# Optimization experiments

Hardware: AMD Instinct MI355X
Metric: run time of the kernel (lower is better)

## Reference

```python
import jax, jax.numpy as jnp
import numpy as np

B, S, D, H = 4, 2048, 512, 8
HD = D // H
POOL_HEADS = 8


def setup_inputs() -> dict:
    key = jax.random.key(0)
    ks = iter(jax.random.split(key, 32))
    p = {}
    p['x'] = jax.random.normal(next(ks), (B, S, D), dtype=jnp.float32)
    p['mask'] = jnp.zeros((B, S), dtype=jnp.float32)  # key_padding_mask (1.0 = padded)
    s = 1.0 / np.sqrt(D)
    for layer in ('1', '2'):
        for name in ('q', 'k', 'v', 'o'):
            p[f'{name}{layer}_w'] = jax.random.normal(next(ks), (D, D), dtype=jnp.float32) * s
            p[f'{name}{layer}_b'] = jnp.zeros((D,), dtype=jnp.float32)
    p['ln1_g'] = jnp.ones((D,), jnp.float32); p['ln1_b'] = jnp.zeros((D,), jnp.float32)
    p['ffn_w1'] = jax.random.normal(next(ks), (D, D), dtype=jnp.float32) * s
    p['ffn_b1'] = jnp.zeros((D,), jnp.float32)
    p['ffn_w2'] = jax.random.normal(next(ks), (D, D), dtype=jnp.float32) * s
    p['ffn_b2'] = jnp.zeros((D,), jnp.float32)
    p['ln2_g'] = jnp.ones((D,), jnp.float32); p['ln2_b'] = jnp.zeros((D,), jnp.float32)
    p['pool_w'] = jax.random.normal(next(ks), (D, POOL_HEADS), dtype=jnp.float32) * s
    p['pool_b'] = jnp.zeros((POOL_HEADS,), jnp.float32)
    return p


def _layernorm(x, g, b, eps=1e-5):
    mu = jnp.mean(x, axis=-1, keepdims=True)
    var = jnp.var(x, axis=-1, keepdims=True)
    return (x - mu) * jax.lax.rsqrt(var + eps) * g + b


def _mha(x, mask, qw, qb, kw, kb, vw, vb, ow, ob):
    b, s, d = x.shape
    q = (x @ qw + qb).reshape(b, s, H, HD)
    k = (x @ kw + kb).reshape(b, s, H, HD)
    v = (x @ vw + vb).reshape(b, s, H, HD)
    scores = jnp.einsum('bihd,bjhd->bhij', q, k) / jnp.sqrt(jnp.float32(HD))
    scores = scores - mask[:, None, None, :] * 1e30  # key_padding_mask
    w = jax.nn.softmax(scores, axis=-1)  # dropout is identity at eval
    out = jnp.einsum('bhij,bjhd->bihd', w, v).reshape(b, s, d)
    return out @ ow + ob


def _pool(x, mask, pw, pb):
    alpha = jax.nn.leaky_relu(x @ pw + pb)            # [B,S,POOL_HEADS]
    alpha = alpha + mask[:, :, None] * -1e16
    alpha = jax.nn.softmax(alpha, axis=1)             # softmax over sequence
    # sum over heads of alpha_h * x, then sum over sequence
    return jnp.einsum('bs,bsd->bd', alpha.sum(axis=-1), x)


def reference(x, mask,
              q1_w, q1_b, k1_w, k1_b, v1_w, v1_b, o1_w, o1_b,
              q2_w, q2_b, k2_w, k2_b, v2_w, v2_b, o2_w, o2_b,
              ln1_g, ln1_b, ffn_w1, ffn_b1, ffn_w2, ffn_b2,
              ln2_g, ln2_b, pool_w, pool_b):
    # F.normalize(x, p=2, dim=-1)
    x = x / jnp.maximum(jnp.linalg.norm(x, axis=-1, keepdims=True), 1e-12)
    h = _mha(x, mask, q1_w, q1_b, k1_w, k1_b, v1_w, v1_b, o1_w, o1_b)
    h = _layernorm(h, ln1_g, ln1_b)
    h = jax.nn.relu(h @ ffn_w1 + ffn_b1) @ ffn_w2 + ffn_b2
    h = _mha(h, mask, q2_w, q2_b, k2_w, k2_b, v2_w, v2_b, o2_w, o2_b)
    h = _layernorm(h, ln2_g, ln2_b)
    return _pool(h, mask, pool_w, pool_b)  # [B, D] patch_feature (cls=False -> logit is None)
```

## Files before the change

kernel.cpp:

```cpp
#include <hip/hip_runtime.h>
#include <hip/hip_bf16.h>
#include <stdint.h>

#define DEVI __device__ __forceinline__

typedef float f32x4 __attribute__((ext_vector_type(4)));
typedef short bf16x8 __attribute__((ext_vector_type(8)));

typedef __attribute__((address_space(3))) unsigned int as3_u32;
typedef __attribute__((address_space(1))) unsigned int as1_u32;

DEVI void gload16(const void* g, void* l) {
  __builtin_amdgcn_global_load_lds((const as1_u32*)g, (as3_u32*)l, 16, 0, 0);
}

DEVI unsigned short bf16r(float f) {
  union { float f; unsigned int u; } v; v.f = f;
  unsigned int u = v.u;
  return (unsigned short)((u + 0x7FFFu + ((u >> 16) & 1u)) >> 16);
}

DEVI float bf2f(unsigned short u) {
  unsigned int x = ((unsigned int)u) << 16;
  union { unsigned int u; float f; } v; v.u = x;
  return v.f;
}

struct PrepArgs {
  const float* w[10];
  const float* b1[3];
  const float* b2[3];
};

__global__ __launch_bounds__(256) void prep_kernel(PrepArgs pa, unsigned short* wt,
                                                   float* qb1, float* qb2) {
  __shared__ float lt[64][65];
  const int slot = blockIdx.z;
  const int n0 = blockIdx.x * 64, k0 = blockIdx.y * 64;
  const float* W = pa.w[slot];
  for (int it = 0; it < 16; it++) {
    int idx = it * 256 + threadIdx.x;
    int kr = idx >> 6, nc = idx & 63;
    lt[kr][nc] = W[(long)(k0 + kr) * 512 + n0 + nc];
  }
  __syncthreads();
  unsigned short* dst = wt + (long)slot * 512 * 512;
  for (int it = 0; it < 16; it++) {
    int idx = it * 256 + threadIdx.x;
    int nr = idx >> 6, kc = idx & 63;
    dst[(long)(n0 + nr) * 512 + k0 + kc] = bf16r(lt[kc][nr]);
  }
  if (blockIdx.x == 0 && blockIdx.y == 0) {
    if (slot < 3) {
      for (int i = threadIdx.x; i < 512; i += 256) qb1[slot * 512 + i] = pa.b1[slot][i];
    } else if (slot >= 6 && slot < 9) {
      for (int i = threadIdx.x; i < 512; i += 256) qb2[(slot - 6) * 512 + i] = pa.b2[slot - 6][i];
    }
  }
}

__global__ __launch_bounds__(256) void l2norm_kernel(const float* __restrict__ x,
                                                     unsigned short* __restrict__ xn) {
  const long row = blockIdx.x;
  const float* xr = x + row * 512;
  float v0 = xr[threadIdx.x], v1 = xr[threadIdx.x + 256];
  float ss = v0 * v0 + v1 * v1;
  #pragma unroll
  for (int off = 32; off > 0; off >>= 1) ss += __shfl_down(ss, off, 64);
  __shared__ float red[4];
  __shared__ float sc[1];
  int w = threadIdx.x >> 6, ln = threadIdx.x & 63;
  if (ln == 0) red[w] = ss;
  __syncthreads();
  if (threadIdx.x == 0) {
    float S = red[0] + red[1] + red[2] + red[3];
    sc[0] = 1.0f / fmaxf(sqrtf(S), 1e-12f);
  }
  __syncthreads();
  float s = sc[0];
  xn[row * 512 + threadIdx.x] = bf16r(v0 * s);
  xn[row * 512 + threadIdx.x + 256] = bf16r(v1 * s);
}

template <int EPI>
__global__ __launch_bounds__(256) void gemm_bt(const unsigned short* __restrict__ A,
                                               const unsigned short* __restrict__ Bt,
                                               const float* __restrict__ bias,
                                               void* __restrict__ Cv, int K, int N,
                                               unsigned short* __restrict__ vtout) {
  __shared__ unsigned short ldsA[128 * 64];
  __shared__ unsigned short ldsB[128 * 64];
  const int tid = threadIdx.x, w = tid >> 6, ln = tid & 63;
  const int bm = blockIdx.x, bn = blockIdx.y;
  const int wm = (w >> 1) * 64, wn = (w & 1) * 64;
  const f32x4 zf = {0.f, 0.f, 0.f, 0.f};
  f32x4 acc[4][4];
  #pragma unroll
  for (int i = 0; i < 4; i++)
    #pragma unroll
    for (int j = 0; j < 4; j++) acc[i][j] = zf;
  const int r8 = ln >> 3, s8 = ln & 7;
  for (int kt = 0; kt < K; kt += 64) {
    #pragma unroll
    for (int i = 0; i < 4; i++) {
      int row = w * 32 + i * 8 + r8;
      gload16(A + (long)(bm * 128 + row) * K + kt + s8 * 8, &ldsA[(w * 32 + i * 8) * 64]);
      gload16(Bt + (long)(bn * 128 + row) * K + kt + s8 * 8, &ldsB[(w * 32 + i * 8) * 64]);
    }
    __syncthreads();
    #pragma unroll
    for (int kk = 0; kk < 2; kk++) {
      bf16x8 af[4], bfr[4];
      #pragma unroll
      for (int mf = 0; mf < 4; mf++) {
        int row = wm + mf * 16 + (ln & 15);
        af[mf] = *(const bf16x8*)&ldsA[row * 64 + kk * 32 + (ln >> 4) * 8];
      }
      #pragma unroll
      for (int nf = 0; nf < 4; nf++) {
        int row = wn + nf * 16 + (ln & 15);
        bfr[nf] = *(const bf16x8*)&ldsB[row * 64 + kk * 32 + (ln >> 4) * 8];
      }
      #pragma unroll
      for (int mf = 0; mf < 4; mf++)
        #pragma unroll
        for (int nf = 0; nf < 4; nf++)
          acc[mf][nf] = __builtin_amdgcn_mfma_f32_16x16x32_bf16(af[mf], bfr[nf], acc[mf][nf], 0, 0, 0);
    }
    __syncthreads();
  }
  const int g = ln >> 4, c = ln & 15;
  #pragma unroll
  for (int mf = 0; mf < 4; mf++) {
    #pragma unroll
    for (int nf = 0; nf < 4; nf++) {
      int col = bn * 128 + wn + nf * 16 + c;
      float bv = bias[col];
      if (EPI == 3 && col >= 1024) {
        long row0 = bm * 128 + wm + mf * 16 + g * 4;
        int b = (int)(row0 >> 11), s = (int)(row0 & 2047);
        int vc = col - 1024, h = vc >> 6, hd = vc & 63;
        ushort4 o;
        o.x = bf16r(acc[mf][nf][0] + bv);
        o.y = bf16r(acc[mf][nf][1] + bv);
        o.z = bf16r(acc[mf][nf][2] + bv);
        o.w = bf16r(acc[mf][nf][3] + bv);
        *(ushort4*)(vtout + ((long)((b * 8 + h) * 64 + hd)) * 2048 + s) = o;
      } else {
        #pragma unroll
        for (int j = 0; j < 4; j++) {
          long row = bm * 128 + wm + mf * 16 + g * 4 + j;
          float v = acc[mf][nf][j] + bv;
          if (EPI == 2) v = v > 0.f ? v : 0.f;
          if (EPI == 0)
            ((float*)Cv)[row * N + col] = v;
          else
            ((unsigned short*)Cv)[row * N + col] = bf16r(v);
        }
      }
    }
  }
}

template <int EPI>
__global__ __launch_bounds__(256) void gemm_bt64(const unsigned short* __restrict__ A,
                                                 const unsigned short* __restrict__ Bt,
                                                 const float* __restrict__ bias,
                                                 void* __restrict__ Cv, int K, int N) {
  __shared__ unsigned short ldsA[128 * 64];
  __shared__ unsigned short ldsB[64 * 64];
  const int tid = threadIdx.x, w = tid >> 6, ln = tid & 63;
  const int bm = blockIdx.x, bn = blockIdx.y;
  const int wm = (w >> 1) * 64, wn = (w & 1) * 32;
  const f32x4 zf = {0.f, 0.f, 0.f, 0.f};
  f32x4 acc[4][2];
  #pragma unroll
  for (int i = 0; i < 4; i++)
    #pragma unroll
    for (int j = 0; j < 2; j++) acc[i][j] = zf;
  const int r8 = ln >> 3, s8 = ln & 7;
  for (int kt = 0; kt < K; kt += 64) {
    #pragma unroll
    for (int i = 0; i < 6; i++) {
      int jj = w * 6 + i;
      if (jj < 16) {
        gload16(A + (long)(bm * 128 + jj * 8 + r8) * K + kt + s8 * 8, &ldsA[jj * 512]);
      } else {
        int jb = jj - 16;
        gload16(Bt + (long)(bn * 64 + jb * 8 + r8) * K + kt + s8 * 8, &ldsB[jb * 512]);
      }
    }
    __syncthreads();
    #pragma unroll
    for (int kk = 0; kk < 2; kk++) {
      bf16x8 af[4], bfr[2];
      #pragma unroll
      for (int mf = 0; mf < 4; mf++)
        af[mf] = *(const bf16x8*)&ldsA[(wm + mf * 16 + (ln & 15)) * 64 + kk * 32 + (ln >> 4) * 8];
      #pragma unroll
      for (int nf = 0; nf < 2; nf++)
        bfr[nf] = *(const bf16x8*)&ldsB[(wn + nf * 16 + (ln & 15)) * 64 + kk * 32 + (ln >> 4) * 8];
      #pragma unroll
      for (int mf = 0; mf < 4; mf++)
        #pragma unroll
        for (int nf = 0; nf < 2; nf++)
          acc[mf][nf] = __builtin_amdgcn_mfma_f32_16x16x32_bf16(af[mf], bfr[nf], acc[mf][nf], 0, 0, 0);
    }
    __syncthreads();
  }
  const int g = ln >> 4, c = ln & 15;
  #pragma unroll
  for (int mf = 0; mf < 4; mf++) {
    #pragma unroll
    for (int nf = 0; nf < 2; nf++) {
      int col = bn * 64 + wn + nf * 16 + c;
      float bv = bias[col];
      #pragma unroll
      for (int j = 0; j < 4; j++) {
        long row = bm * 128 + wm + mf * 16 + g * 4 + j;
        float v = acc[mf][nf][j] + bv;
        if (EPI == 2) v = v > 0.f ? v : 0.f;
        if (EPI == 0)
          ((float*)Cv)[row * N + col] = v;
        else
          ((unsigned short*)Cv)[row * N + col] = bf16r(v);
      }
    }
  }
}

__global__ __launch_bounds__(256, 4) void attn_split_kernel(
    const unsigned short* __restrict__ qkv,
    const unsigned short* __restrict__ vt,
    const float* __restrict__ mask,
    unsigned short* __restrict__ opart,
    float* __restrict__ lpart) {
  const int tid = threadIdx.x, w = tid >> 6, ln = tid & 63;
  const int g = ln >> 4, c = ln & 15;
  const int bh = blockIdx.y, b = bh >> 3, h = bh & 7;
  const int sp = blockIdx.z;
  const int q0 = blockIdx.x * 128 + w * 32;
  const unsigned short* qp = qkv + (long)(b * 2048) * 1536 + h * 64;
  const unsigned short* kp = qp + 512;
  const unsigned short* vtp = vt + (long)bh * 64 * 2048;
  const float* mp = mask + b * 2048;

  __shared__ unsigned short kbuf[2][32 * 64];
  __shared__ unsigned short vbuf[2][64 * 32];
  __shared__ unsigned short pbuf[4 * 16 * 64];
  unsigned short* pb = &pbuf[w * 1024];

  const int jj0 = w * 2;
  auto stage = [&](int buf, int kt) {
    #pragma unroll
    for (int u = 0; u < 2; u++) {
      int jj = jj0 + u;
      if (jj < 4) {
        int r = jj * 8 + (ln >> 3);
        int s = ln & 7;
        gload16(kp + (long)(kt + r) * 1536 + ((s ^ (r & 7)) * 8),
                &kbuf[buf][jj * 512]);
      } else {
        int j = jj - 4;
        int r = j * 16 + (ln >> 2);
        int s = ln & 3;
        gload16(vtp + (long)r * 2048 + kt + ((s ^ ((r >> 1) & 3)) * 8),
                &vbuf[buf][j * 512]);
      }
    }
  };

  const f32x4 zf = {0.f, 0.f, 0.f, 0.f};
  bf16x8 qf[2][2];
  #pragma unroll
  for (int qi = 0; qi < 2; qi++)
    #pragma unroll
    for (int kk = 0; kk < 2; kk++)
      qf[qi][kk] = *(const bf16x8*)(qp + (long)(q0 + qi * 16 + c) * 1536 + kk * 32 + g * 8);

  f32x4 of[4][2];
  #pragma unroll
  for (int i = 0; i < 4; i++)
    #pragma unroll
    for (int j = 0; j < 2; j++) of[i][j] = zf;
  float lsum[2] = {0.f, 0.f};

  const int kt0 = sp * 1024;
  stage(0, kt0);
  __syncthreads();

  for (int it = 0; it < 32; it++) {
    const int kt = kt0 + it * 32;
    const int cur = it & 1;
    if (it + 1 < 32) stage(cur ^ 1, kt + 32);
    float mval = mp[kt + (ln & 31)];
    bf16x8 kf[2][2];
    #pragma unroll
    for (int ki = 0; ki < 2; ki++)
      #pragma unroll
      for (int kk = 0; kk < 2; kk++)
        kf[ki][kk] = *(const bf16x8*)&kbuf[cur][(ki * 16 + c) * 64 + (((kk * 4 + g) ^ (c & 7)) * 8)];
    bf16x8 vf[4];
    #pragma unroll
    for (int hf = 0; hf < 4; hf++)
      vf[hf] = *(const bf16x8*)&vbuf[cur][(hf * 16 + c) * 32 + ((g ^ ((c >> 1) & 3)) * 8)];
    f32x4 st[2][2];
    #pragma unroll
    for (int ki = 0; ki < 2; ki++)
      #pragma unroll
      for (int qi = 0; qi < 2; qi++) {
        f32x4 t0 = __builtin_amdgcn_mfma_f32_16x16x32_bf16(kf[ki][0], qf[qi][0], zf, 0, 0, 0);
        st[ki][qi] = __builtin_amdgcn_mfma_f32_16x16x32_bf16(kf[ki][1], qf[qi][1], t0, 0, 0, 0);
      }
    float madj[2][4];
    #pragma unroll
    for (int ki = 0; ki < 2; ki++)
      #pragma unroll
      for (int j = 0; j < 4; j++) madj[ki][j] = 0.f;
    if (__any(mval != 0.f)) {
      #pragma unroll
      for (int ki = 0; ki < 2; ki++)
        #pragma unroll
        for (int j = 0; j < 4; j++)
          madj[ki][j] = -1.4426950408889634e30f * __shfl(mval, ki * 16 + g * 4 + j, 64);
    }
    const float SC = 0.18033688011112042f;
    #pragma unroll
    for (int qi = 0; qi < 2; qi++) {
      #pragma unroll
      for (int ki = 0; ki < 2; ki++) {
        float e0 = __builtin_amdgcn_exp2f(st[ki][qi][0] * SC + madj[ki][0]);
        float e1 = __builtin_amdgcn_exp2f(st[ki][qi][1] * SC + madj[ki][1]);
        float e2 = __builtin_amdgcn_exp2f(st[ki][qi][2] * SC + madj[ki][2]);
        float e3 = __builtin_amdgcn_exp2f(st[ki][qi][3] * SC + madj[ki][3]);
        lsum[qi] += (e0 + e1) + (e2 + e3);
        __hip_bfloat162 h01 = __float22bfloat162_rn(make_float2(e0, e1));
        __hip_bfloat162 h23 = __float22bfloat162_rn(make_float2(e2, e3));
        uint2 pk;
        pk.x = *(unsigned int*)&h01;
        pk.y = *(unsigned int*)&h23;
        int slot = (qi * 4 + ki * 2 + (g >> 1)) ^ (c & 7);
        *(uint2*)&pb[c * 64 + slot * 8 + (g & 1) * 4] = pk;
      }
    }
    bf16x8 pfr[2];
    #pragma unroll
    for (int qi = 0; qi < 2; qi++) {
      int slot = (qi * 4 + g) ^ (c & 7);
      pfr[qi] = *(const bf16x8*)&pb[c * 64 + slot * 8];
    }
    #pragma unroll
    for (int hf = 0; hf < 4; hf++)
      #pragma unroll
      for (int qi = 0; qi < 2; qi++)
        of[hf][qi] = __builtin_amdgcn_mfma_f32_16x16x32_bf16(vf[hf], pfr[qi], of[hf][qi], 0, 0, 0);
    __syncthreads();
  }
  #pragma unroll
  for (int qi = 0; qi < 2; qi++) {
    lsum[qi] += __shfl_xor(lsum[qi], 16, 64);
    lsum[qi] += __shfl_xor(lsum[qi], 32, 64);
  }
  unsigned short* ob = opart + (long)(sp * 32 + bh) * 2048 * 64;
  #pragma unroll
  for (int qi = 0; qi < 2; qi++) {
    long row = q0 + qi * 16 + c;
    #pragma unroll
    for (int hf = 0; hf < 4; hf++) {
      ushort4 o;
      o.x = bf16r(of[hf][qi][0]);
      o.y = bf16r(of[hf][qi][1]);
      o.z = bf16r(of[hf][qi][2]);
      o.w = bf16r(of[hf][qi][3]);
      *(ushort4*)(ob + row * 64 + hf * 16 + g * 4) = o;
    }
  }
  if (g == 0) {
    #pragma unroll
    for (int qi = 0; qi < 2; qi++)
      lpart[(long)(sp * 32 + bh) * 2048 + q0 + qi * 16 + c] = lsum[qi];
  }
}

__global__ __launch_bounds__(256) void attn_combine(const unsigned short* __restrict__ opart,
                                                    const float* __restrict__ lpart,
                                                    unsigned short* __restrict__ ao) {
  const long row = blockIdx.x;
  const int b = (int)(row >> 11), q = (int)(row & 2047);
  #pragma unroll
  for (int half = 0; half < 2; half++) {
    int col = threadIdx.x + half * 256;
    int h = col >> 6, hd = col & 63;
    int bh = b * 8 + h;
    float l = lpart[(long)bh * 2048 + q] + lpart[(long)(32 + bh) * 2048 + q];
    long i0 = ((long)bh * 2048 + q) * 64 + hd;
    long i1 = ((long)(32 + bh) * 2048 + q) * 64 + hd;
    float v = (bf2f(opart[i0]) + bf2f(opart[i1])) / l;
    ao[row * 512 + col] = bf16r(v);
  }
}

template <int OUTF>
__global__ __launch_bounds__(256) void ln_kernel(const float* __restrict__ in,
                                                 const float* __restrict__ gam,
                                                 const float* __restrict__ bet,
                                                 void* __restrict__ out) {
  const long row = blockIdx.x;
  const float* x = in + row * 512;
  float v0 = x[threadIdx.x], v1 = x[threadIdx.x + 256];
  float s = v0 + v1, ss = v0 * v0 + v1 * v1;
  #pragma unroll
  for (int off = 32; off > 0; off >>= 1) {
    s += __shfl_down(s, off, 64);
    ss += __shfl_down(ss, off, 64);
  }
  __shared__ float red[8];
  __shared__ float mv[2];
  int w = threadIdx.x >> 6, ln = threadIdx.x & 63;
  if (ln == 0) { red[w] = s; red[w + 4] = ss; }
  __syncthreads();
  if (threadIdx.x == 0) {
    float S = red[0] + red[1] + red[2] + red[3];
    float SS = red[4] + red[5] + red[6] + red[7];
    float mu = S * (1.f / 512.f);
    float var = SS * (1.f / 512.f) - mu * mu;
    mv[0] = mu;
    mv[1] = rsqrtf(var + 1e-5f);
  }
  __syncthreads();
  float mu = mv[0], rs = mv[1];
  float o0 = (v0 - mu) * rs * gam[threadIdx.x] + bet[threadIdx.x];
  float o1 = (v1 - mu) * rs * gam[threadIdx.x + 256] + bet[threadIdx.x + 256];
  if (OUTF == 0) {
    ((unsigned short*)out)[row * 512 + threadIdx.x] = bf16r(o0);
    ((unsigned short*)out)[row * 512 + threadIdx.x + 256] = bf16r(o1);
  } else {
    ((float*)out)[row * 512 + threadIdx.x] = o0;
    ((float*)out)[row * 512 + threadIdx.x + 256] = o1;
  }
}

__global__ __launch_bounds__(256) void alpha_kernel(const float* __restrict__ h,
                                                    const float* __restrict__ pw,
                                                    const float* __restrict__ pbias,
                                                    const float* __restrict__ mask,
                                                    float* __restrict__ alpha) {
  int w = threadIdx.x >> 6, ln = threadIdx.x & 63;
  long row = (long)blockIdx.x * 4 + w;
  float p[8];
  #pragma unroll
  for (int k = 0; k < 8; k++) p[k] = 0.f;
  #pragma unroll
  for (int it = 0; it < 8; it++) {
    int d = it * 64 + ln;
    float xv = h[row * 512 + d];
    const float* wr = pw + d * 8;
    #pragma unroll
    for (int k = 0; k < 8; k++) p[k] += xv * wr[k];
  }
  #pragma unroll
  for (int off = 32; off > 0; off >>= 1)
    #pragma unroll
    for (int k = 0; k < 8; k++) p[k] += __shfl_down(p[k], off, 64);
  if (ln == 0) {
    float mterm = mask[row] * (-1e16f);
    #pragma unroll
    for (int k = 0; k < 8; k++) {
      float a = p[k] + pbias[k];
      a = a < 0.f ? 0.01f * a : a;
      alpha[row * 8 + k] = a + mterm;
    }
  }
}

__global__ __launch_bounds__(256) void stats_kernel(const float* __restrict__ alpha,
                                                    float* __restrict__ stats) {
  int b = blockIdx.x >> 3, ph = blockIdx.x & 7;
  const float* a = alpha + (long)b * 2048 * 8 + ph;
  __shared__ float rr[4];
  __shared__ float mm[1];
  int w = threadIdx.x >> 6, ln = threadIdx.x & 63;
  float m = -1e38f;
  for (int s = threadIdx.x; s < 2048; s += 256) m = fmaxf(m, a[(long)s * 8]);
  #pragma unroll
  for (int off = 32; off > 0; off >>= 1) m = fmaxf(m, __shfl_down(m, off, 64));
  if (ln == 0) rr[w] = m;
  __syncthreads();
  if (threadIdx.x == 0) mm[0] = fmaxf(fmaxf(rr[0], rr[1]), fmaxf(rr[2], rr[3]));
  __syncthreads();
  float M = mm[0];
  float sum = 0.f;
  for (int s = threadIdx.x; s < 2048; s += 256) sum += __expf(a[(long)s * 8] - M);
  #pragma unroll
  for (int off = 32; off > 0; off >>= 1) sum += __shfl_down(sum, off, 64);
  __syncthreads();
  if (ln == 0) rr[w] = sum;
  __syncthreads();
  if (threadIdx.x == 0) {
    stats[blockIdx.x * 2] = M;
    stats[blockIdx.x * 2 + 1] = rr[0] + rr[1] + rr[2] + rr[3];
  }
}

__global__ __launch_bounds__(256) void pool_kernel(const float* __restrict__ h,
                                                   const float* __restrict__ alpha,
                                                   const float* __restrict__ stats,
                                                   float* __restrict__ partial) {
  int b = blockIdx.x >> 3, sc = blockIdx.x & 7;
  int s0 = sc * 256;
  __shared__ float wb[256];
  {
    long s = s0 + threadIdx.x;
    const float* a = alpha + ((long)b * 2048 + s) * 8;
    float wsum = 0.f;
    #pragma unroll
    for (int ph = 0; ph < 8; ph++) {
      float M = stats[(b * 8 + ph) * 2], Sm = stats[(b * 8 + ph) * 2 + 1];
      wsum += __expf(a[ph] - M) / Sm;
    }
    wb[threadIdx.x] = wsum;
  }
  __syncthreads();
  float a0 = 0.f, a1 = 0.f;
  const float* hb = h + ((long)b * 2048 + s0) * 512;
  for (int i = 0; i < 256; i++) {
    float wv = wb[i];
    a0 += wv * hb[(long)i * 512 + threadIdx.x];
    a1 += wv * hb[(long)i * 512 + threadIdx.x + 256];
  }
  partial[(long)blockIdx.x * 512 + threadIdx.x] = a0;
  partial[(long)blockIdx.x * 512 + threadIdx.x + 256] = a1;
}

__global__ __launch_bounds__(256) void pool_final(const float* __restrict__ partial,
                                                  float* __restrict__ out) {
  int b = blockIdx.x;
  float a0 = 0.f, a1 = 0.f;
  #pragma unroll
  for (int sc = 0; sc < 8; sc++) {
    a0 += partial[(long)(b * 8 + sc) * 512 + threadIdx.x];
    a1 += partial[(long)(b * 8 + sc) * 512 + threadIdx.x + 256];
  }
  out[b * 512 + threadIdx.x] = a0;
  out[b * 512 + threadIdx.x + 256] = a1;
}

extern "C" void kernel_launch(void* const* d_in, const int* in_sizes, int n_in,
                              void* d_out, int out_size, void* d_ws, size_t ws_size,
                              hipStream_t stream) {
  (void)in_sizes; (void)n_in; (void)out_size;
  if (ws_size < 92274688UL) return;

  const float* x    = (const float*)d_in[0];
  const float* mask = (const float*)d_in[1];
  const float* q1w = (const float*)d_in[2];  const float* q1b = (const float*)d_in[3];
  const float* k1w = (const float*)d_in[4];  const float* k1b = (const float*)d_in[5];
  const float* v1w = (const float*)d_in[6];  const float* v1b = (const float*)d_in[7];
  const float* o1w = (const float*)d_in[8];  const float* o1b = (const float*)d_in[9];
  const float* q2w = (const float*)d_in[10]; const float* q2b = (const float*)d_in[11];
  const float* k2w = (const float*)d_in[12]; const float* k2b = (const float*)d_in[13];
  const float* v2w = (const float*)d_in[14]; const float* v2b = (const float*)d_in[15];
  const float* o2w = (const float*)d_in[16]; const float* o2b = (const float*)d_in[17];
  const float* ln1g = (const float*)d_in[18]; const float* ln1b = (const float*)d_in[19];
  const float* fw1 = (const float*)d_in[20]; const float* fb1 = (const float*)d_in[21];
  const float* fw2 = (const float*)d_in[22]; const float* fb2 = (const float*)d_in[23];
  const float* ln2g = (const float*)d_in[24]; const float* ln2b = (const float*)d_in[25];
  const float* poolw = (const float*)d_in[26]; const float* poolb = (const float*)d_in[27];

  char* ws = (char*)d_ws;
  unsigned short* Wt  = (unsigned short*)(ws + 0);
  float* qb1          = (float*)(ws + 5242880);
  float* qb2          = (float*)(ws + 5249024);
  float* stats        = (float*)(ws + 5255168);
  float* alpha        = (float*)(ws + 5255424);
  float* partial      = (float*)(ws + 5517568);
  unsigned short* qkv = (unsigned short*)(ws + 8388608);
  unsigned short* vt  = (unsigned short*)(ws + 33554432);
  unsigned short* ao  = (unsigned short*)(ws + 41943040);
  float* t            = (float*)(ws + 50331648);
  unsigned short* xn  = (unsigned short*)(ws + 67108864);
  unsigned short* h1  = (unsigned short*)(ws + 75497472);
  unsigned short* f   = (unsigned short*)(ws + 83886080);
  unsigned short* h2  = xn;
  unsigned short* opart = (unsigned short*)(ws + 50331648);
  float* lpart          = (float*)(ws + 83886080);

  PrepArgs pa;
  pa.w[0] = q1w; pa.w[1] = k1w; pa.w[2] = v1w; pa.w[3] = o1w; pa.w[4] = fw1;
  pa.w[5] = fw2; pa.w[6] = q2w; pa.w[7] = k2w; pa.w[8] = v2w; pa.w[9] = o2w;
  pa.b1[0] = q1b; pa.b1[1] = k1b; pa.b1[2] = v1b;
  pa.b2[0] = q2b; pa.b2[1] = k2b; pa.b2[2] = v2b;

  prep_kernel<<<dim3(8, 8, 10), 256, 0, stream>>>(pa, Wt, qb1, qb2);
  l2norm_kernel<<<8192, 256, 0, stream>>>(x, xn);

  gemm_bt<3><<<dim3(64, 12), 256, 0, stream>>>(xn, Wt, qb1, qkv, 512, 1536, vt);
  attn_split_kernel<<<dim3(16, 32, 2), 256, 0, stream>>>(qkv, vt, mask, opart, lpart);
  attn_combine<<<8192, 256, 0, stream>>>(opart, lpart, ao);
  gemm_bt64<0><<<dim3(64, 8), 256, 0, stream>>>(ao, Wt + 3L * 512 * 512, o1b, t, 512, 512);
  ln_kernel<0><<<8192, 256, 0, stream>>>(t, ln1g, ln1b, h1);
  gemm_bt64<2><<<dim3(64, 8), 256, 0, stream>>>(h1, Wt + 4L * 512 * 512, fb1, f, 512, 512);
  gemm_bt64<1><<<dim3(64, 8), 256, 0, stream>>>(f, Wt + 5L * 512 * 512, fb2, h2, 512, 512);

  gemm_bt<3><<<dim3(64, 12), 256, 0, stream>>>(h2, Wt + 6L * 512 * 512, qb2, qkv, 512, 1536, vt);
  attn_split_kernel<<<dim3(16, 32, 2), 256, 0, stream>>>(qkv, vt, mask, opart, lpart);
  attn_combine<<<8192, 256, 0, stream>>>(opart, lpart, ao);
  gemm_bt64<0><<<dim3(64, 8), 256, 0, stream>>>(ao, Wt + 9L * 512 * 512, o2b, t, 512, 512);
  ln_kernel<1><<<8192, 256, 0, stream>>>(t, ln2g, ln2b, t);

  alpha_kernel<<<2048, 256, 0, stream>>>(t, poolw, poolb, mask, alpha);
  stats_kernel<<<32, 256, 0, stream>>>(alpha, stats);
  pool_kernel<<<32, 256, 0, stream>>>(t, alpha, stats, partial);
  pool_final<<<4, 256, 0, stream>>>(partial, (float*)d_out);
}
```

Measured before the change: 302.8 us.

## Switch split attention to 32x32x16 MFMA with register P exchange and block swizzle

Rewrites the attention inner loop to use 32x32x16 bf16 MFMA tiles instead of 16x16x32 ones, so each wave computes a 32x32 score tile in four MFMAs. The softmax probabilities are moved into B-operand layout with cross-half lane shuffles instead of a round trip through the per-wave LDS P buffer, which removes that shared memory and its writes and reads. It also remaps block IDs so consecutive blocks spread across heads and splits, which may improve L2 locality. The cost is larger accumulator register footprint (two 16-wide accumulators plus the score tile), which may pressure occupancy under the 4-block launch bound.

New measurement: 306.9 us. Within noise of the previous version (+1.3%).

```diff
diff --git a/kernel.cpp b/kernel.cpp
--- a/kernel.cpp
+++ b/kernel.cpp
@@ -5,6 +5,7 @@
 #define DEVI __device__ __forceinline__
 
 typedef float f32x4 __attribute__((ext_vector_type(4)));
+typedef float f32x16 __attribute__((ext_vector_type(16)));
 typedef short bf16x8 __attribute__((ext_vector_type(8)));
 
 typedef __attribute__((address_space(3))) unsigned int as3_u32;
@@ -24,6 +25,11 @@
   unsigned int x = ((unsigned int)u) << 16;
   union { unsigned int u; float f; } v; v.u = x;
   return v.f;
+}
+
+DEVI unsigned int pkbf16(float a, float b) {
+  __hip_bfloat162 h = __float22bfloat162_rn(make_float2(a, b));
+  return *(unsigned int*)&h;
 }
 
 struct PrepArgs {
@@ -236,10 +242,12 @@
     unsigned short* __restrict__ opart,
     float* __restrict__ lpart) {
   const int tid = threadIdx.x, w = tid >> 6, ln = tid & 63;
-  const int g = ln >> 4, c = ln & 15;
-  const int bh = blockIdx.y, b = bh >> 3, h = bh & 7;
-  const int sp = blockIdx.z;
-  const int q0 = blockIdx.x * 128 + w * 32;
+  const int lo = ln & 31, hi = ln >> 5;
+  const int bid = blockIdx.x + 16 * blockIdx.y + 512 * blockIdx.z;
+  const int swz = (bid & 7) * 128 + (bid >> 3);
+  const int qb = swz & 15, bh = (swz >> 4) & 31, sp = swz >> 9;
+  const int b = bh >> 3, h = bh & 7;
+  const int q0 = qb * 128 + w * 32;
   const unsigned short* qp = qkv + (long)(b * 2048) * 1536 + h * 64;
   const unsigned short* kp = qp + 512;
   const unsigned short* vtp = vt + (long)bh * 64 * 2048;
@@ -247,8 +255,6 @@
 
   __shared__ unsigned short kbuf[2][32 * 64];
   __shared__ unsigned short vbuf[2][64 * 32];
-  __shared__ unsigned short pbuf[4 * 16 * 64];
-  unsigned short* pb = &pbuf[w * 1024];
 
   const int jj0 = w * 2;
   auto stage = [&](int buf, int kt) {
@@ -270,20 +276,18 @@
     }
   };
 
-  const f32x4 zf = {0.f, 0.f, 0.f, 0.f};
-  bf16x8 qf[2][2];
-  #pragma unroll
-  for (int qi = 0; qi < 2; qi++)
-    #pragma unroll
-    for (int kk = 0; kk < 2; kk++)
-      qf[qi][kk] = *(const bf16x8*)(qp + (long)(q0 + qi * 16 + c) * 1536 + kk * 32 + g * 8);
-
-  f32x4 of[4][2];
-  #pragma unroll
-  for (int i = 0; i < 4; i++)
-    #pragma unroll
-    for (int j = 0; j < 2; j++) of[i][j] = zf;
-  float lsum[2] = {0.f, 0.f};
+  bf16x8 qf[4];
+  #pragma unroll
+  for (int t = 0; t < 4; t++)
+    qf[t] = *(const bf16x8*)(qp + (long)(q0 + lo) * 1536 + t * 16 + hi * 8);
+
+  f32x16 oacc[2];
+  #pragma unroll
+  for (int t = 0; t < 2; t++)
+    #pragma unroll
+    for (int r = 0; r < 16; r++) oacc[t][r] = 0.f;
+  float lsum = 0.f;
+  const f32x16 zf16 = oacc[0];
 
   const int kt0 = sp * 1024;
   stage(0, kt0);
@@ -293,93 +297,69 @@
     const int kt = kt0 + it * 32;
     const int cur = it & 1;
     if (it + 1 < 32) stage(cur ^ 1, kt + 32);
-    float mval = mp[kt + (ln & 31)];
-    bf16x8 kf[2][2];
-    #pragma unroll
-    for (int ki = 0; ki < 2; ki++)
-      #pragma unroll
-      for (int kk = 0; kk < 2; kk++)
-        kf[ki][kk] = *(const bf16x8*)&kbuf[cur][(ki * 16 + c) * 64 + (((kk * 4 + g) ^ (c & 7)) * 8)];
-    bf16x8 vf[4];
-    #pragma unroll
-    for (int hf = 0; hf < 4; hf++)
-      vf[hf] = *(const bf16x8*)&vbuf[cur][(hf * 16 + c) * 32 + ((g ^ ((c >> 1) & 3)) * 8)];
-    f32x4 st[2][2];
-    #pragma unroll
-    for (int ki = 0; ki < 2; ki++)
-      #pragma unroll
-      for (int qi = 0; qi < 2; qi++) {
-        f32x4 t0 = __builtin_amdgcn_mfma_f32_16x16x32_bf16(kf[ki][0], qf[qi][0], zf, 0, 0, 0);
-        st[ki][qi] = __builtin_amdgcn_mfma_f32_16x16x32_bf16(kf[ki][1], qf[qi][1], t0, 0, 0, 0);
-      }
-    float madj[2][4];
-    #pragma unroll
-    for (int ki = 0; ki < 2; ki++)
-      #pragma unroll
-      for (int j = 0; j < 4; j++) madj[ki][j] = 0.f;
+    float mval = mp[kt + lo];
+    f32x16 sacc = zf16;
+    #pragma unroll
+    for (int t = 0; t < 4; t++) {
+      bf16x8 kf = *(const bf16x8*)&kbuf[cur][lo * 64 + (((t * 2 + hi) ^ (lo & 7)) * 8)];
+      sacc = __builtin_amdgcn_mfma_f32_32x32x16_bf16(kf, qf[t], sacc, 0, 0, 0);
+    }
+    const float SC = 0.18033688011112042f;
+    float e[16];
     if (__any(mval != 0.f)) {
       #pragma unroll
-      for (int ki = 0; ki < 2; ki++)
-        #pragma unroll
-        for (int j = 0; j < 4; j++)
-          madj[ki][j] = -1.4426950408889634e30f * __shfl(mval, ki * 16 + g * 4 + j, 64);
-    }
-    const float SC = 0.18033688011112042f;
-    #pragma unroll
-    for (int qi = 0; qi < 2; qi++) {
-      #pragma unroll
-      for (int ki = 0; ki < 2; ki++) {
-        float e0 = __builtin_amdgcn_exp2f(st[ki][qi][0] * SC + madj[ki][0]);
-        float e1 = __builtin_amdgcn_exp2f(st[ki][qi][1] * SC + madj[ki][1]);
-        float e2 = __builtin_amdgcn_exp2f(st[ki][qi][2] * SC + madj[ki][2]);
-        float e3 = __builtin_amdgcn_exp2f(st[ki][qi][3] * SC + madj[ki][3]);
-        lsum[qi] += (e0 + e1) + (e2 + e3);
-        __hip_bfloat162 h01 = __float22bfloat162_rn(make_float2(e0, e1));
-        __hip_bfloat162 h23 = __float22bfloat162_rn(make_float2(e2, e3));
-        uint2 pk;
-        pk.x = *(unsigned int*)&h01;
-        pk.y = *(unsigned int*)&h23;
-        int slot = (qi * 4 + ki * 2 + (g >> 1)) ^ (c & 7);
-        *(uint2*)&pb[c * 64 + slot * 8 + (g & 1) * 4] = pk;
-      }
-    }
-    bf16x8 pfr[2];
-    #pragma unroll
-    for (int qi = 0; qi < 2; qi++) {
-      int slot = (qi * 4 + g) ^ (c & 7);
-      pfr[qi] = *(const bf16x8*)&pb[c * 64 + slot * 8];
-    }
-    #pragma unroll
-    for (int hf = 0; hf < 4; hf++)
-      #pragma unroll
-      for (int qi = 0; qi < 2; qi++)
-        of[hf][qi] = __builtin_amdgcn_mfma_f32_16x16x32_bf16(vf[hf], pfr[qi], of[hf][qi], 0, 0, 0);
+      for (int r = 0; r < 16; r++) {
+        float mk = __shfl(mval, (r & 3) + 8 * (r >> 2) + 4 * hi, 64);
+        e[r] = __builtin_amdgcn_exp2f(sacc[r] * SC - 1.4426950408889634e30f * mk);
+      }
+    } else {
+      #pragma unroll
+      for (int r = 0; r < 16; r++)
+        e[r] = __builtin_amdgcn_exp2f(sacc[r] * SC);
+    }
+    #pragma unroll
+    for (int r = 0; r < 16; r++) lsum += e[r];
+    unsigned int cv[8];
+    #pragma unroll
+    for (int i = 0; i < 8; i++) cv[i] = pkbf16(e[2 * i], e[2 * i + 1]);
+    #pragma unroll
+    for (int stt = 0; stt < 2; stt++) {
+      unsigned int c0 = cv[stt * 4 + 0], c1 = cv[stt * 4 + 1];
+      unsigned int c2 = cv[stt * 4 + 2], c3 = cv[stt * 4 + 3];
+      unsigned int s0 = __shfl_xor(c0, 32, 64), s1 = __shfl_xor(c1, 32, 64);
+      unsigned int s2 = __shfl_xor(c2, 32, 64), s3 = __shfl_xor(c3, 32, 64);
+      unsigned int pf[4];
+      pf[0] = hi ? s2 : c0;
+      pf[1] = hi ? s3 : c1;
+      pf[2] = hi ? c2 : s0;
+      pf[3] = hi ? c3 : s1;
+      bf16x8 pfr = *(const bf16x8*)pf;
+      #pragma unroll
+      for (int tau = 0; tau < 2; tau++) {
+        int vr = tau * 32 + lo;
+        bf16x8 vf = *(const bf16x8*)&vbuf[cur][vr * 32 + ((((stt * 2 + hi) ^ ((vr >> 1) & 3))) * 8)];
+        oacc[tau] = __builtin_amdgcn_mfma_f32_32x32x16_bf16(vf, pfr, oacc[tau], 0, 0, 0);
+      }
+    }
     __syncthreads();
   }
-  #pragma unroll
-  for (int qi = 0; qi < 2; qi++) {
-    lsum[qi] += __shfl_xor(lsum[qi], 16, 64);
-    lsum[qi] += __shfl_xor(lsum[qi], 32, 64);
-  }
+  lsum += __shfl_xor(lsum, 32, 64);
   unsigned short* ob = opart + (long)(sp * 32 + bh) * 2048 * 64;
-  #pragma unroll
-  for (int qi = 0; qi < 2; qi++) {
-    long row = q0 + qi * 16 + c;
-    #pragma unroll
-    for (int hf = 0; hf < 4; hf++) {
+  const long row = q0 + lo;
+  #pragma unroll
+  for (int tau = 0; tau < 2; tau++) {
+    #pragma unroll
+    for (int j = 0; j < 4; j++) {
       ushort4 o;
-      o.x = bf16r(of[hf][qi][0]);
-      o.y = bf16r(of[hf][qi][1]);
-      o.z = bf16r(of[hf][qi][2]);
-      o.w = bf16r(of[hf][qi][3]);
-      *(ushort4*)(ob + row * 64 + hf * 16 + g * 4) = o;
-    }
-  }
-  if (g == 0) {
-    #pragma unroll
-    for (int qi = 0; qi < 2; qi++)
-      lpart[(long)(sp * 32 + bh) * 2048 + q0 + qi * 16 + c] = lsum[qi];
-  }
+      o.x = bf16r(oacc[tau][4 * j + 0]);
+      o.y = bf16r(oacc[tau][4 * j + 1]);
+      o.z = bf16r(oacc[tau][4 * j + 2]);
+      o.w = bf16r(oacc[tau][4 * j + 3]);
+      *(ushort4*)(ob + row * 64 + tau * 32 + j * 8 + hi * 4) = o;
+    }
+  }
+  if (hi == 0)
+    lpart[(long)(sp * 32 + bh) * 2048 + row] = lsum;
 }
 
 __global__ __launch_bounds__(256) void attn_combine(const unsigned short* __restrict__ opart,
```
